# Optimization experiments

Hardware: AMD Instinct MI355X
Metric: run time of the kernel (lower is better)

## Reference

```python
import jax, jax.numpy as jnp
import numpy as np

B, N, C = 2, 4096, 512
NUM_HEADS = 8
HEAD_DIM = C // NUM_HEADS
SCALE = HEAD_DIM ** -0.5
THETA = 10000.0


def setup_inputs() -> dict:
    key = jax.random.key(0)
    ks = jax.random.split(key, 5)
    x = jax.random.normal(ks[0], (B, N, C), dtype=jnp.float32)
    Wqkv = jax.random.normal(ks[1], (3 * C, C), dtype=jnp.float32) * 0.02
    bqkv = jax.random.normal(ks[2], (3 * C,), dtype=jnp.float32) * 0.02
    Wproj = jax.random.normal(ks[3], (C, C), dtype=jnp.float32) * 0.02
    bproj = jax.random.normal(ks[4], (C,), dtype=jnp.float32) * 0.02
    return {"x": x, "Wqkv": Wqkv, "bqkv": bqkv, "Wproj": Wproj, "bproj": bproj}


def _rope(x, seq_len, head_dim):
    # x: [B, H, N, head_dim]; interleaved rotary embedding
    freqs = 1.0 / THETA ** (jnp.arange(0, head_dim, 2, dtype=jnp.float32) / head_dim)  # [hd/2]
    t = jnp.arange(seq_len, dtype=jnp.float32)
    freqs_cis = jnp.outer(t, freqs)                      # [N, hd/2]
    sin_f = jnp.sin(freqs_cis)
    cos_f = jnp.cos(freqs_cis)
    x_even = x[..., ::2]                                 # [B, H, N, hd/2]
    x_odd = x[..., 1::2]
    rot = jnp.stack(
        [x_even * cos_f - x_odd * sin_f,
         x_even * sin_f + x_odd * cos_f],
        axis=-1,
    )                                                    # [B, H, N, hd/2, 2]
    return rot.reshape(x.shape)


def reference(x, Wqkv, bqkv, Wproj, bproj):
    b, n, c = x.shape
    # fused QKV projection: y = x @ W.T + b
    qkv = x @ Wqkv.T + bqkv                              # [B, N, 3C]
    qkv = qkv.reshape(b, n, 3, NUM_HEADS, HEAD_DIM)
    qkv = jnp.transpose(qkv, (2, 0, 3, 1, 4))            # [3, B, H, N, hd]
    q, k, v = qkv[0], qkv[1], qkv[2]
    q = _rope(q, n, HEAD_DIM)
    k = _rope(k, n, HEAD_DIM)
    attn = jnp.einsum('bhqd,bhkd->bhqk', q, k) * SCALE   # [B, H, N, N]
    attn = jax.nn.softmax(attn, axis=-1)
    out = jnp.einsum('bhqk,bhkd->bhqd', attn, v)         # [B, H, N, hd]
    out = jnp.transpose(out, (0, 2, 1, 3)).reshape(b, n, c)
    return out @ Wproj.T + bproj
```

## Files before the change

kernel.cpp:

```cpp
#include <hip/hip_runtime.h>
#include <hip/hip_bf16.h>
#include <stdint.h>

#define B_ 2
#define N_ 4096
#define C_ 512
#define H_ 8
#define D_ 64
#define M_ (B_*N_)
#define K3_ (3*C_)
#define NCH 2

typedef __attribute__((ext_vector_type(8)))  short short8;
typedef __attribute__((ext_vector_type(4)))  float f32x4;
typedef __attribute__((ext_vector_type(16))) float f32x16;

static __device__ __forceinline__ unsigned short f2bf(float f) {
  union { float f; unsigned u; } cv; cv.f = f;
  unsigned r = cv.u + 0x7fffu + ((cv.u >> 16) & 1u);
  return (unsigned short)(r >> 16);
}
static __device__ __forceinline__ float bf2f(short x) {
  union { unsigned u; float f; } cv;
  cv.u = ((unsigned)(unsigned short)x) << 16;
  return cv.f;
}
static __device__ __forceinline__ float fexp2(float x) {
#if __has_builtin(__builtin_amdgcn_exp2f)
  return __builtin_amdgcn_exp2f(x);
#else
  return exp2f(x);
#endif
}
static __device__ __forceinline__ unsigned cvt_pk_bf16(float a, float b) {
  unsigned r;
  asm("v_cvt_pk_bf16_f32 %0, %1, %2" : "=v"(r) : "v"(a), "v"(b));
  return r;
}
static __device__ __forceinline__ void gload_lds16(const void* g, void* l) {
  __builtin_amdgcn_global_load_lds((const __attribute__((address_space(1))) unsigned*)g,
                                   (__attribute__((address_space(3))) unsigned*)l, 16, 0, 0);
}
static __device__ __forceinline__ f32x16 zero16() {
  f32x16 z;
#pragma unroll
  for (int i = 0; i < 16; i++) z[i] = 0.f;
  return z;
}

__global__ void prep(const float* __restrict__ x, const float* __restrict__ Wqkv,
                     const float* __restrict__ Wproj,
                     short* __restrict__ xb, short* __restrict__ wqkvb,
                     short* __restrict__ wprjb, float2* __restrict__ tab) {
  int blk = blockIdx.x, t = threadIdx.x;
  if (blk < 4096) {
    int i = blk * 256 + t;
    float4 v = ((const float4*)x)[i];
    short4 o;
    o.x = (short)f2bf(v.x); o.y = (short)f2bf(v.y);
    o.z = (short)f2bf(v.z); o.w = (short)f2bf(v.w);
    ((short4*)xb)[i] = o;
  } else if (blk < 4864) {
    int i = (blk - 4096) * 256 + t;
    float4 v = ((const float4*)Wqkv)[i];
    short4 o;
    o.x = (short)f2bf(v.x); o.y = (short)f2bf(v.y);
    o.z = (short)f2bf(v.z); o.w = (short)f2bf(v.w);
    ((short4*)wqkvb)[i] = o;
  } else if (blk < 5120) {
    int i = (blk - 4864) * 256 + t;
    float4 v = ((const float4*)Wproj)[i];
    short4 o;
    o.x = (short)f2bf(v.x); o.y = (short)f2bf(v.y);
    o.z = (short)f2bf(v.z); o.w = (short)f2bf(v.w);
    ((short4*)wprjb)[i] = o;
  } else {
    int i = (blk - 5120) * 256 + t;
    int p = i & 31, n = i >> 5;
    float freq = exp2f(-((float)(2 * p) / 64.0f) * 13.287712379549449f);
    float ang = (float)n * freq;
    float s, c;
    sincosf(ang, &s, &c);
    float2 r; r.x = c; r.y = s;
    tab[i] = r;
  }
}

__global__ void rope_vt(const short* __restrict__ qkvb, const float2* __restrict__ tab,
                        short* __restrict__ Qf, short* __restrict__ Kf,
                        short* __restrict__ Vf) {
  __shared__ short tile[128][72];
  int blk = blockIdx.x, t = threadIdx.x;
  if (blk < 1024) {
    int tk = blk >> 9;
    int bh = (blk & 511) >> 5;
    int nb4 = blk & 31;
    int b = bh >> 3, h = bh & 7;
    int n0 = nb4 * 128;
#pragma unroll
    for (int pass = 0; pass < 4; pass++) {
      int row = pass * 32 + (t >> 3), chunk = t & 7;
      short8 v = *(const short8*)(qkvb + (size_t)(b * N_ + n0 + row) * K3_ + tk * C_ + h * D_ + chunk * 8);
      *(short8*)&tile[row][chunk * 8] = v;
    }
    __syncthreads();
    int lane = t & 63, f = t >> 6;
    int c = lane & 31, hi = lane >> 5;
    int d0 = f * 16 + hi * 8;
    float sc = (tk == 0) ? 0.18033688011112042f : 1.0f;
    short* base = (tk ? Kf : Qf);
#pragma unroll
    for (int i = 0; i < 4; i++) {
      int n_l = i * 32 + c;
      short8 v = *(const short8*)&tile[n_l][d0];
      const float2* tp = tab + (size_t)(n0 + n_l) * 32 + (d0 >> 1);
      short8 w;
#pragma unroll
      for (int j = 0; j < 4; j++) {
        float e = bf2f(v[2 * j]), o = bf2f(v[2 * j + 1]);
        float2 cs = tp[j];
        float e2 = (e * cs.x - o * cs.y) * sc;
        float o2 = (e * cs.y + o * cs.x) * sc;
        w[2 * j] = (short)f2bf(e2);
        w[2 * j + 1] = (short)f2bf(o2);
      }
      short* dst = base + (((size_t)(bh * 128 + nb4 * 4 + i) * 4 + f) * 512) + lane * 8;
      *(short8*)dst = w;
    }
  } else {
    int blk2 = blk - 1024;
    int bh = blk2 >> 7, kblk = blk2 & 127;
    int b = bh >> 3, h = bh & 7;
    int n0 = kblk * 32;
    {
      int row = t >> 3, c8 = t & 7;
      short8 v = *(const short8*)(qkvb + (size_t)(b * N_ + n0 + row) * K3_ + 2 * C_ + h * D_ + c8 * 8);
      *(short8*)&tile[row][c8 * 8] = v;
    }
    __syncthreads();
    {
      int frag = t >> 6, lane = t & 63;
      int hi = lane >> 5, c = lane & 31;
      int g = frag & 1, dblk = frag >> 1;
      short8 w;
#pragma unroll
      for (int j = 0; j < 8; j++) w[j] = tile[g * 16 + hi * 8 + j][dblk * 32 + c];
      *(short8*)(Vf + ((size_t)(bh * 128 + kblk) * 4 + frag) * 512 + lane * 8) = w;
    }
  }
}

template<int OUTF32, int MFR>
__global__ __launch_bounds__(256) void gemm_bt(const short* __restrict__ A, const short* __restrict__ Bw,
                                               const float* __restrict__ bias, void* __restrict__ Cout,
                                               int M, int Nout, int K) {
  __shared__ short As[MFR * 32 * 64];
  __shared__ short Bs[128 * 64];
  int t = threadIdx.x, lane = t & 63, w = t >> 6, wr = w >> 1, wc = w & 1;
  int tM = blockIdx.x * (MFR * 32), tN = blockIdx.y * 128;
  int lrow = lane & 15, lhi = lane >> 4;
  int rs = (lrow & 7) * 8;
  f32x4 acc[MFR][4];
#pragma unroll
  for (int fm = 0; fm < MFR; fm++)
#pragma unroll
    for (int fn = 0; fn < 4; fn++)
#pragma unroll
      for (int r = 0; r < 4; r++) acc[fm][fn][r] = 0.f;

  int srow = t >> 3;
  int sq = ((t & 7) * 8) ^ ((srow & 7) * 8);

  for (int k0 = 0; k0 < K; k0 += 64) {
#pragma unroll
    for (int p = 0; p < MFR; p++)
      gload_lds16(A + (size_t)(tM + p * 32 + srow) * K + k0 + sq, As + p * 2048 + t * 8);
#pragma unroll
    for (int p = 0; p < 4; p++)
      gload_lds16(Bw + (size_t)(tN + p * 32 + srow) * K + k0 + sq, Bs + p * 2048 + t * 8);
    __syncthreads();
#pragma unroll
    for (int kk = 0; kk < 2; kk++) {
      int ko = (kk * 32 + lhi * 8) ^ rs;
      short8 af[MFR], bfr[4];
#pragma unroll
      for (int f = 0; f < MFR; f++)
        af[f] = *(const short8*)(As + (wr * (MFR * 16) + f * 16 + lrow) * 64 + ko);
#pragma unroll
      for (int f = 0; f < 4; f++)
        bfr[f] = *(const short8*)(Bs + (wc * 64 + f * 16 + lrow) * 64 + ko);
#pragma unroll
      for (int fm = 0; fm < MFR; fm++)
#pragma unroll
        for (int fn = 0; fn < 4; fn++)
          acc[fm][fn] = __builtin_amdgcn_mfma_f32_16x16x32_bf16(af[fm], bfr[fn], acc[fm][fn], 0, 0, 0);
    }
    __syncthreads();
  }

#pragma unroll
  for (int fn = 0; fn < 4; fn++) {
    int col = tN + wc * 64 + fn * 16 + lrow;
    float bv = bias[col];
#pragma unroll
    for (int fm = 0; fm < MFR; fm++) {
      int row0 = tM + wr * (MFR * 16) + fm * 16 + lhi * 4;
#pragma unroll
      for (int r = 0; r < 4; r++) {
        float v = acc[fm][fn][r] + bv;
        if (OUTF32) ((float*)Cout)[(size_t)(row0 + r) * Nout + col] = v;
        else        ((short*)Cout)[(size_t)(row0 + r) * Nout + col] = (short)f2bf(v);
      }
    }
  }
}

static __device__ __forceinline__ f32x16 qk4(const short8* k, const short8* q, const f32x16& z0) {
  __builtin_amdgcn_s_setprio(1);
  f32x16 st = __builtin_amdgcn_mfma_f32_32x32x16_bf16(k[0], q[0], z0, 0, 0, 0);
  st = __builtin_amdgcn_mfma_f32_32x32x16_bf16(k[1], q[1], st, 0, 0, 0);
  st = __builtin_amdgcn_mfma_f32_32x32x16_bf16(k[2], q[2], st, 0, 0, 0);
  st = __builtin_amdgcn_mfma_f32_32x32x16_bf16(k[3], q[3], st, 0, 0, 0);
  __builtin_amdgcn_s_setprio(0);
  return st;
}
static __device__ __forceinline__ void soft_pv(const f32x16& st, const short8* v, const short8& ones,
                                               f32x16& o0, f32x16& o1, f32x16& o2) {
  unsigned cpk[8];
#pragma unroll
  for (int q2 = 0; q2 < 4; q2++) {
    float e0 = fexp2(st[4 * q2]),     e1 = fexp2(st[4 * q2 + 1]);
    float e2 = fexp2(st[4 * q2 + 2]), e3 = fexp2(st[4 * q2 + 3]);
    cpk[2 * q2]     = cvt_pk_bf16(e0, e1);
    cpk[2 * q2 + 1] = cvt_pk_bf16(e2, e3);
  }
  unsigned w00 = cpk[0], w02 = cpk[2];
  asm volatile("v_permlane32_swap_b32 %0, %1" : "+v"(w00), "+v"(w02));
  unsigned w01 = cpk[1], w03 = cpk[3];
  asm volatile("v_permlane32_swap_b32 %0, %1" : "+v"(w01), "+v"(w03));
  unsigned w10 = cpk[4], w12 = cpk[6];
  asm volatile("v_permlane32_swap_b32 %0, %1" : "+v"(w10), "+v"(w12));
  unsigned w11 = cpk[5], w13 = cpk[7];
  asm volatile("v_permlane32_swap_b32 %0, %1" : "+v"(w11), "+v"(w13));
  union { unsigned u[4]; short8 s; } u0, u1;
  u0.u[0] = w00; u0.u[1] = w01; u0.u[2] = w02; u0.u[3] = w03;
  u1.u[0] = w10; u1.u[1] = w11; u1.u[2] = w12; u1.u[3] = w13;
  __builtin_amdgcn_s_setprio(1);
  o0 = __builtin_amdgcn_mfma_f32_32x32x16_bf16(u0.s, v[0], o0, 0, 0, 0);
  o0 = __builtin_amdgcn_mfma_f32_32x32x16_bf16(u1.s, v[1], o0, 0, 0, 0);
  o1 = __builtin_amdgcn_mfma_f32_32x32x16_bf16(u0.s, v[2], o1, 0, 0, 0);
  o1 = __builtin_amdgcn_mfma_f32_32x32x16_bf16(u1.s, v[3], o1, 0, 0, 0);
  o2 = __builtin_amdgcn_mfma_f32_32x32x16_bf16(u0.s, ones, o2, 0, 0, 0);
  o2 = __builtin_amdgcn_mfma_f32_32x32x16_bf16(u1.s, ones, o2, 0, 0, 0);
  __builtin_amdgcn_s_setprio(0);
}

__global__ __launch_bounds__(256, 4) void attn(const short* __restrict__ Qf, const short* __restrict__ Kf,
                                               const short* __restrict__ Vf,
                                               short* __restrict__ Op, float* __restrict__ lp) {
  __shared__ short Ks[2][4096];
  __shared__ short Vs[2][4096];
  int bh = blockIdx.x;
  int ch = blockIdx.z;
  int t = threadIdx.x;
  int wv = t >> 6, lane = t & 63;
  int c = lane & 31, hi = lane >> 5;
  int q0 = blockIdx.y * 128 + wv * 32;
  const int nkb2 = N_ / (NCH * 64);
  int kb0 = ch * (N_ / (NCH * 32));

  const short* Qb = Qf + ((size_t)(bh * 128 + (q0 >> 5)) * 4) * 512 + lane * 8;
  const short* Kg = Kf + ((size_t)(bh * 128 + kb0) * 4) * 512 + t * 8;
  const short* Vg = Vf + ((size_t)(bh * 128 + kb0) * 4) * 512 + t * 8;

  short8 qf4[4];
#pragma unroll
  for (int f = 0; f < 4; f++) qf4[f] = *(const short8*)(Qb + f * 512);

  short8 ones;
#pragma unroll
  for (int j = 0; j < 8; j++) ones[j] = (short)0x3F80;

  const f32x16 z0 = zero16();
  f32x16 o0 = z0, o1 = z0, o2 = z0;

  gload_lds16(Kg,        &Ks[0][t * 8]);
  gload_lds16(Kg + 2048, &Ks[0][2048 + t * 8]);
  gload_lds16(Vg,        &Vs[0][t * 8]);
  gload_lds16(Vg + 2048, &Vs[0][2048 + t * 8]);
  __syncthreads();

  int buf = 0;
  for (int it = 0; it < nkb2; ++it) {
    if (it + 1 < nkb2) {
      const short* Kn = Kg + (size_t)(it + 1) * 4096;
      const short* Vn = Vg + (size_t)(it + 1) * 4096;
      gload_lds16(Kn,        &Ks[buf ^ 1][t * 8]);
      gload_lds16(Kn + 2048, &Ks[buf ^ 1][2048 + t * 8]);
      gload_lds16(Vn,        &Vs[buf ^ 1][t * 8]);
      gload_lds16(Vn + 2048, &Vs[buf ^ 1][2048 + t * 8]);
    }
#pragma unroll
    for (int s = 0; s < 2; s++) {
      short8 kf[4], vf[4];
#pragma unroll
      for (int f = 0; f < 4; f++) kf[f] = *(const short8*)&Ks[buf][s * 2048 + f * 512 + lane * 8];
#pragma unroll
      for (int f = 0; f < 4; f++) vf[f] = *(const short8*)&Vs[buf][s * 2048 + f * 512 + lane * 8];
      f32x16 st = qk4(kf, qf4, z0);
      soft_pv(st, vf, ones, o0, o1, o2);
    }
    __syncthreads();
    buf ^= 1;
  }

  if (c == 0) {
    float* lrow = lp + ((size_t)ch * 16 + bh) * N_ + q0;
#pragma unroll
    for (int r = 0; r < 16; r++) lrow[(r & 3) + 8 * (r >> 2) + 4 * hi] = o2[r];
  }
  short* obase = Op + ((size_t)ch * 16 + bh) * N_ * D_;
#pragma unroll
  for (int r = 0; r < 16; r++) {
    int ql = (r & 3) + 8 * (r >> 2) + 4 * hi;
    int n = q0 + ql;
    obase[(size_t)n * D_ + c]      = (short)f2bf(o0[r]);
    obase[(size_t)n * D_ + 32 + c] = (short)f2bf(o1[r]);
  }
}

__global__ void combine(const short* __restrict__ Op, const float* __restrict__ lp,
                        short* __restrict__ AO) {
  int i = blockIdx.x * blockDim.x + threadIdx.x;
  if (i >= 16 * N_ * 8) return;
  int d8 = i & 7, q = (i >> 3) & (N_ - 1), bh = i >> 15;
  const size_t chs = (size_t)16 * N_ * D_;
  size_t base = ((size_t)bh * N_ + q) * D_ + d8 * 8;
  float acc[8];
#pragma unroll
  for (int j = 0; j < 8; j++) acc[j] = 0.f;
  float l = 0.f;
#pragma unroll
  for (int chv = 0; chv < NCH; chv++) {
    short8 v = *(const short8*)(Op + chv * chs + base);
#pragma unroll
    for (int j = 0; j < 8; j++) acc[j] += bf2f(v[j]);
    l += lp[((size_t)chv * 16 + bh) * N_ + q];
  }
  float inv = 1.0f / l;
  int bb = bh >> 3, h = bh & 7;
  short8 o;
#pragma unroll
  for (int j = 0; j < 8; j++) o[j] = (short)f2bf(acc[j] * inv);
  *(short8*)(AO + ((size_t)(bb * N_ + q)) * C_ + h * D_ + d8 * 8) = o;
}

extern "C" void kernel_launch(void* const* d_in, const int* in_sizes, int n_in,
                              void* d_out, int out_size, void* d_ws, size_t ws_size,
                              hipStream_t stream) {
  const float* x     = (const float*)d_in[0];
  const float* Wqkv  = (const float*)d_in[1];
  const float* bqkv  = (const float*)d_in[2];
  const float* Wproj = (const float*)d_in[3];
  const float* bproj = (const float*)d_in[4];
  float* out = (float*)d_out;
  char* ws = (char*)d_ws;

  const size_t off_wprjb = 0;
  const size_t off_tab   = 524288;
  const size_t off_q     = 1572864;
  const size_t off_k     = 9961472;
  const size_t off_vt    = 18350080;
  const size_t off_ao    = 26738688;
  const size_t off_xb    = 35127296;
  const size_t off_wqkvb = 43515904;
  const size_t off_qkvb  = 45088768;
  const size_t off_op    = 35127296;
  const size_t off_l     = 68681728;
  if (ws_size < 70254592) return;

  short* xb    = (short*)(ws + off_xb);
  short* wqkvb = (short*)(ws + off_wqkvb);
  short* wprjb = (short*)(ws + off_wprjb);
  short* qkvb  = (short*)(ws + off_qkvb);
  short* Qfp   = (short*)(ws + off_q);
  short* Kfp   = (short*)(ws + off_k);
  short* Vfp   = (short*)(ws + off_vt);
  short* AOp   = (short*)(ws + off_ao);
  float2* tab  = (float2*)(ws + off_tab);
  short* Opp   = (short*)(ws + off_op);
  float* lpp   = (float*)(ws + off_l);

  prep<<<dim3(5632), dim3(256), 0, stream>>>(x, Wqkv, Wproj, xb, wqkvb, wprjb, tab);

  gemm_bt<0, 4><<<dim3(64, 12), dim3(256), 0, stream>>>(xb, wqkvb, bqkv, qkvb, M_, K3_, C_);

  rope_vt<<<dim3(3072), dim3(256), 0, stream>>>(qkvb, tab, Qfp, Kfp, Vfp);

  attn<<<dim3(16, 32, NCH), dim3(256), 0, stream>>>(Qfp, Kfp, Vfp, Opp, lpp);
  combine<<<dim3(2048), dim3(256), 0, stream>>>(Opp, lpp, AOp);

  gemm_bt<1, 2><<<dim3(128, 4), dim3(256), 0, stream>>>(AOp, wprjb, bproj, (void*)out, M_, C_, C_);
}
```

Measured before the change: 141.0 us.

## Process two 32-row query tiles per wave to reuse K/V LDS fragments

Each wave in the attention kernel now handles 64 query rows (two 32-row Q tiles) instead of 32, so each K/V fragment read from LDS feeds twice as many MFMAs. The grid is halved along the query dimension and launch bounds drop from 4 to 2 blocks per CU to allow for the doubled accumulator and Q register use. This cuts LDS traffic and global K/V loads per query, at the cost of higher register pressure, lower occupancy and fewer blocks (512) to spread across the CUs.

After: 134.5 us. 4.6% less time.

```diff
diff --git a/kernel.cpp b/kernel.cpp
--- a/kernel.cpp
+++ b/kernel.cpp
@@ -255,7 +255,7 @@
   __builtin_amdgcn_s_setprio(0);
 }
 
-__global__ __launch_bounds__(256, 4) void attn(const short* __restrict__ Qf, const short* __restrict__ Kf,
+__global__ __launch_bounds__(256, 2) void attn(const short* __restrict__ Qf, const short* __restrict__ Kf,
                                                const short* __restrict__ Vf,
                                                short* __restrict__ Op, float* __restrict__ lp) {
   __shared__ short Ks[2][4096];
@@ -265,24 +265,27 @@
   int t = threadIdx.x;
   int wv = t >> 6, lane = t & 63;
   int c = lane & 31, hi = lane >> 5;
-  int q0 = blockIdx.y * 128 + wv * 32;
+  int q0 = blockIdx.y * 256 + wv * 64;
   const int nkb2 = N_ / (NCH * 64);
   int kb0 = ch * (N_ / (NCH * 32));
 
-  const short* Qb = Qf + ((size_t)(bh * 128 + (q0 >> 5)) * 4) * 512 + lane * 8;
+  const short* QbA = Qf + ((size_t)(bh * 128 + (q0 >> 5)) * 4) * 512 + lane * 8;
   const short* Kg = Kf + ((size_t)(bh * 128 + kb0) * 4) * 512 + t * 8;
   const short* Vg = Vf + ((size_t)(bh * 128 + kb0) * 4) * 512 + t * 8;
 
-  short8 qf4[4];
-#pragma unroll
-  for (int f = 0; f < 4; f++) qf4[f] = *(const short8*)(Qb + f * 512);
+  short8 qA[4], qB[4];
+#pragma unroll
+  for (int f = 0; f < 4; f++) qA[f] = *(const short8*)(QbA + f * 512);
+#pragma unroll
+  for (int f = 0; f < 4; f++) qB[f] = *(const short8*)(QbA + (4 + f) * 512);
 
   short8 ones;
 #pragma unroll
   for (int j = 0; j < 8; j++) ones[j] = (short)0x3F80;
 
   const f32x16 z0 = zero16();
-  f32x16 o0 = z0, o1 = z0, o2 = z0;
+  f32x16 oA0 = z0, oA1 = z0, oA2 = z0;
+  f32x16 oB0 = z0, oB1 = z0, oB2 = z0;
 
   gload_lds16(Kg,        &Ks[0][t * 8]);
   gload_lds16(Kg + 2048, &Ks[0][2048 + t * 8]);
@@ -307,25 +310,34 @@
       for (int f = 0; f < 4; f++) kf[f] = *(const short8*)&Ks[buf][s * 2048 + f * 512 + lane * 8];
 #pragma unroll
       for (int f = 0; f < 4; f++) vf[f] = *(const short8*)&Vs[buf][s * 2048 + f * 512 + lane * 8];
-      f32x16 st = qk4(kf, qf4, z0);
-      soft_pv(st, vf, ones, o0, o1, o2);
+      f32x16 stA = qk4(kf, qA, z0);
+      f32x16 stB = qk4(kf, qB, z0);
+      soft_pv(stA, vf, ones, oA0, oA1, oA2);
+      soft_pv(stB, vf, ones, oB0, oB1, oB2);
     }
     __syncthreads();
     buf ^= 1;
   }
 
+  float* lrow = lp + ((size_t)ch * 16 + bh) * N_ + q0;
+  short* obase = Op + ((size_t)ch * 16 + bh) * N_ * D_;
   if (c == 0) {
-    float* lrow = lp + ((size_t)ch * 16 + bh) * N_ + q0;
-#pragma unroll
-    for (int r = 0; r < 16; r++) lrow[(r & 3) + 8 * (r >> 2) + 4 * hi] = o2[r];
-  }
-  short* obase = Op + ((size_t)ch * 16 + bh) * N_ * D_;
+#pragma unroll
+    for (int r = 0; r < 16; r++) {
+      int ql = (r & 3) + 8 * (r >> 2) + 4 * hi;
+      lrow[ql] = oA2[r];
+      lrow[32 + ql] = oB2[r];
+    }
+  }
 #pragma unroll
   for (int r = 0; r < 16; r++) {
     int ql = (r & 3) + 8 * (r >> 2) + 4 * hi;
-    int n = q0 + ql;
-    obase[(size_t)n * D_ + c]      = (short)f2bf(o0[r]);
-    obase[(size_t)n * D_ + 32 + c] = (short)f2bf(o1[r]);
+    size_t nA = (size_t)(q0 + ql) * D_;
+    size_t nB = (size_t)(q0 + 32 + ql) * D_;
+    obase[nA + c]      = (short)f2bf(oA0[r]);
+    obase[nA + 32 + c] = (short)f2bf(oA1[r]);
+    obase[nB + c]      = (short)f2bf(oB0[r]);
+    obase[nB + 32 + c] = (short)f2bf(oB1[r]);
   }
 }
 
@@ -397,7 +409,7 @@
 
   rope_vt<<<dim3(3072), dim3(256), 0, stream>>>(qkvb, tab, Qfp, Kfp, Vfp);
 
-  attn<<<dim3(16, 32, NCH), dim3(256), 0, stream>>>(Qfp, Kfp, Vfp, Opp, lpp);
+  attn<<<dim3(16, 16, NCH), dim3(256), 0, stream>>>(Qfp, Kfp, Vfp, Opp, lpp);
   combine<<<dim3(2048), dim3(256), 0, stream>>>(Opp, lpp, AOp);
 
   gemm_bt<1, 2><<<dim3(128, 4), dim3(256), 0, stream>>>(AOp, wprjb, bproj, (void*)out, M_, C_, C_);
```
